# Kernel tuning notes

Measured on AMD Instinct MI355X. Metric: run time of the kernel, lower is better.

The kernel has to match this reference:

```python
import jax, jax.numpy as jnp
import numpy as np

MODEL_DIM = 1024
NUM_HEADS = 16
HEAD_DIM = MODEL_DIM // NUM_HEADS


def setup_inputs() -> dict:
    key = jax.random.key(0)
    ks = jax.random.split(key, 9)
    s = 1.0 / np.sqrt(MODEL_DIM)
    d = {
        "query": jax.random.normal(ks[0], (2, 2048, MODEL_DIM), dtype=jnp.float32),
        "Wq": jax.random.normal(ks[1], (MODEL_DIM, MODEL_DIM), dtype=jnp.float32) * s,
        "bq": jnp.zeros((MODEL_DIM,), dtype=jnp.float32),
        "Wk": jax.random.normal(ks[2], (MODEL_DIM, MODEL_DIM), dtype=jnp.float32) * s,
        "bk": jnp.zeros((MODEL_DIM,), dtype=jnp.float32),
        "Wv": jax.random.normal(ks[3], (MODEL_DIM, MODEL_DIM), dtype=jnp.float32) * s,
        "bv": jnp.zeros((MODEL_DIM,), dtype=jnp.float32),
        "Wo": jax.random.normal(ks[4], (MODEL_DIM, MODEL_DIM), dtype=jnp.float32) * s,
        "bo": jnp.zeros((MODEL_DIM,), dtype=jnp.float32),
    }
    return d


def reference(query, Wq, bq, Wk, bk, Wv, bv, Wo, bo):
    B, S, D = query.shape
    H, hd = NUM_HEADS, HEAD_DIM
    # self-attention: key = value = query
    q = (query @ Wq.T + bq).reshape(B, S, H, hd).transpose(0, 2, 1, 3)  # [B,H,S,hd]
    k = (query @ Wk.T + bk).reshape(B, S, H, hd).transpose(0, 2, 1, 3)
    v = (query @ Wv.T + bv).reshape(B, S, H, hd).transpose(0, 2, 1, 3)
    scores = jnp.einsum("bhqd,bhkd->bhqk", q, k) / np.sqrt(hd)  # [B,H,S,S]
    attn = jax.nn.softmax(scores, axis=-1)
    ctx = jnp.einsum("bhqk,bhkd->bhqd", attn, v)  # [B,H,S,hd]
    ctx = ctx.transpose(0, 2, 1, 3).reshape(B, S, D)
    return ctx @ Wo.T + bo
```

## Files before the change

kernel.cpp:

```cpp
#include <hip/hip_runtime.h>

typedef __attribute__((ext_vector_type(8))) __bf16 bf16x8;
typedef __attribute__((ext_vector_type(8))) unsigned short ushort8;
typedef __attribute__((ext_vector_type(4))) unsigned short ushort4v;
typedef __attribute__((ext_vector_type(4))) float f32x4;
typedef __attribute__((ext_vector_type(4))) _Float16 f16x4;
typedef __attribute__((ext_vector_type(8))) _Float16 f16x8;

__device__ __forceinline__ unsigned short f2bf(float f) {
    union { float f; unsigned int u; } c; c.f = f;
    unsigned int u = c.u;
    u += 0x7fffu + ((u >> 16) & 1u);
    return (unsigned short)(u >> 16);
}

__device__ __forceinline__ void async16(const void* g, void* l) {
    __builtin_amdgcn_global_load_lds(
        (const __attribute__((address_space(1))) unsigned int*)g,
        (__attribute__((address_space(3))) unsigned int*)l, 16, 0, 0);
}

__global__ __launch_bounds__(256) void cvt_all(
    const float* __restrict__ q,  const float* __restrict__ wq,
    const float* __restrict__ wk, const float* __restrict__ wv,
    const float* __restrict__ wo,
    unsigned short* __restrict__ q_bf, unsigned short* __restrict__ wqkv,
    unsigned short* __restrict__ wo_bf, float scale_k)
{
    const int NQ = 4096 * 1024, NW = 1024 * 1024;
    int i = (blockIdx.x * 256 + threadIdx.x) * 4;
    const float* src; unsigned short* dst; float sc = 1.0f; int off;
    if (i < NQ)               { src = q;  dst = q_bf;          off = i; }
    else if (i < NQ + NW)     { src = wq; dst = wqkv;          off = i - NQ; }
    else if (i < NQ + 2 * NW) { src = wk; dst = wqkv + NW;     off = i - NQ - NW; sc = scale_k; }
    else if (i < NQ + 3 * NW) { src = wv; dst = wqkv + 2 * NW; off = i - NQ - 2 * NW; }
    else                      { src = wo; dst = wo_bf;         off = i - NQ - 3 * NW; }
    float4 v = *(const float4*)(src + off);
    ushort4v o;
    o[0] = f2bf(v.x * sc); o[1] = f2bf(v.y * sc);
    o[2] = f2bf(v.z * sc); o[3] = f2bf(v.w * sc);
    *(ushort4v*)(dst + off) = o;
}

template<int MODE>
__global__ __launch_bounds__(256) void gemm_bt(
    const unsigned short* __restrict__ A,
    const unsigned short* __restrict__ B,
    void* __restrict__ Cout,
    const float* __restrict__ b0, const float* __restrict__ b1, const float* __restrict__ b2,
    float s0, float s1, float s2,
    int N, int K, int ksz)
{
    __shared__ __align__(16) unsigned short As[128 * 64];
    __shared__ __align__(16) unsigned short Bs[128 * 64];

    const int tid  = threadIdx.x;
    const int lane = tid & 63, wave = tid >> 6;
    const int quad = lane >> 4, l15 = lane & 15;
    const int wm = wave >> 1, wn = wave & 1;
    const int by = blockIdx.y, bx = blockIdx.x;
    const int k0 = blockIdx.z * ksz;

    const int srow = lane >> 3;
    const int sp   = lane & 7;
    const int scl  = sp ^ srow;
    const int sw   = l15 & 7;

    f32x4 acc[4][4];
#pragma unroll
    for (int i = 0; i < 4; ++i)
#pragma unroll
        for (int j = 0; j < 4; ++j) acc[i][j] = (f32x4)(0.0f);

    const int nk = ksz >> 6;
    for (int kt = 0; kt < nk; ++kt) {
        __syncthreads();
#pragma unroll
        for (int j = 0; j < 4; ++j) {
            int r0 = wave * 32 + j * 8;
            async16(A + (size_t)(by * 128 + r0 + srow) * K + k0 + kt * 64 + scl * 8, &As[r0 * 64]);
            async16(B + (size_t)(bx * 128 + r0 + srow) * K + k0 + kt * 64 + scl * 8, &Bs[r0 * 64]);
        }
        __syncthreads();

#pragma unroll
        for (int kh = 0; kh < 2; ++kh) {
            bf16x8 af[4], bfr[4];
#pragma unroll
            for (int mi = 0; mi < 4; ++mi)
                af[mi] = __builtin_bit_cast(bf16x8,
                    *(const ushort8*)&As[(wm * 64 + mi * 16 + l15) * 64 + ((kh * 4 + quad) ^ sw) * 8]);
#pragma unroll
            for (int ni = 0; ni < 4; ++ni)
                bfr[ni] = __builtin_bit_cast(bf16x8,
                    *(const ushort8*)&Bs[(wn * 64 + ni * 16 + l15) * 64 + ((kh * 4 + quad) ^ sw) * 8]);
#pragma unroll
            for (int mi = 0; mi < 4; ++mi)
#pragma unroll
                for (int ni = 0; ni < 4; ++ni)
                    acc[mi][ni] = __builtin_amdgcn_mfma_f32_16x16x32_bf16(af[mi], bfr[ni], acc[mi][ni], 0, 0, 0);
        }
    }

#pragma unroll
    for (int ni = 0; ni < 4; ++ni) {
        int n = bx * 128 + wn * 64 + ni * 16 + l15;
        float bias = (n < 1024) ? b0[n] * s0 : (n < 2048 ? b1[n - 1024] * s1 : b2[n - 2048] * s2);
        if (MODE == 0 && blockIdx.z != 0) bias = 0.0f;
#pragma unroll
        for (int mi = 0; mi < 4; ++mi) {
#pragma unroll
            for (int r = 0; r < 4; ++r) {
                int m = by * 128 + wm * 64 + mi * 16 + quad * 4 + r;
                float v = acc[mi][ni][r] + bias;
                if (MODE == 1) ((unsigned short*)Cout)[(size_t)m * N + n] = f2bf(v);
                else           unsafeAtomicAdd(&((float*)Cout)[(size_t)m * N + n], v);
            }
        }
    }
}

__global__ __launch_bounds__(256) void transpose_v(const unsigned short* __restrict__ qkv,
                                                   _Float16* __restrict__ vtg)
{
    __shared__ unsigned short Ls[64][68];
    const int tid = threadIdx.x;
    const int bh = blockIdx.y, st = blockIdx.x;
    const int b = bh >> 4, h = bh & 15;

#pragma unroll
    for (int i = 0; i < 2; ++i) {
        int s = tid + i * 256;
        int row = s >> 3, c8 = (s & 7) << 3;
        ushort8 v = *(const ushort8*)(qkv + (size_t)(b * 2048 + st * 64 + row) * 3072 + 2048 + h * 64 + c8);
        *(ushort8*)&Ls[row][c8] = v;
    }
    __syncthreads();
#pragma unroll
    for (int i = 0; i < 2; ++i) {
        int s = tid + i * 256;
        int hd = s >> 3, p = s & 7;
        int cl = p ^ (hd & 7);
        int g = cl >> 2, q = cl & 3;
        f16x8 o;
#pragma unroll
        for (int e = 0; e < 8; ++e) {
            int kv = g * 32 + (e >> 2) * 16 + q * 4 + (e & 3);
            union { float f; unsigned int u; } c;
            c.u = ((unsigned int)Ls[kv][hd]) << 16;
            o[e] = (_Float16)c.f;
        }
        *(f16x8*)(vtg + (size_t)(bh * 64 + hd) * 2048 + st * 64 + p * 8) = o;
    }
}

__global__ __launch_bounds__(256) void attn(const unsigned short* __restrict__ qkv,
                                            const _Float16* __restrict__ vtg,
                                            unsigned short* __restrict__ ctx)
{
    __shared__ __align__(16) unsigned short Ks[64 * 64];
    __shared__ __align__(16) _Float16 Vt[64 * 64];

    const int tid  = threadIdx.x;
    const int lane = tid & 63, wave = tid >> 6;
    const int quad = lane >> 4, l15 = lane & 15;
    const int bh = blockIdx.y;
    const int b = bh >> 4, h = bh & 15;
    const int q0 = blockIdx.x * 64;
    const int qrow = b * 2048 + q0 + wave * 16 + l15;

    const int srow = lane >> 3;
    const int sp   = lane & 7;
    const int scl  = sp ^ srow;
    const int sw   = l15 & 7;

    bf16x8 qf[2];
#pragma unroll
    for (int kh = 0; kh < 2; ++kh)
        qf[kh] = __builtin_bit_cast(bf16x8,
            *(const ushort8*)(qkv + (size_t)qrow * 3072 + h * 64 + kh * 32 + quad * 8));

    f32x4 ot[4];
#pragma unroll
    for (int ht = 0; ht < 4; ++ht) ot[ht] = (f32x4)(0.0f);
    float l_acc = 0.0f;

    for (int kt = 0; kt < 32; ++kt) {
        __syncthreads();
#pragma unroll
        for (int i = 0; i < 2; ++i) {
            int row = i * 32 + wave * 8 + srow;
            async16(qkv + (size_t)(b * 2048 + kt * 64 + row) * 3072 + 1024 + h * 64 + scl * 8,
                    &Ks[(i * 32 + wave * 8) * 64]);
            async16(vtg + (size_t)(bh * 64 + row) * 2048 + kt * 64 + sp * 8,
                    (unsigned short*)&Vt[(i * 32 + wave * 8) * 64]);
        }
        __syncthreads();

        f16x4 pv[4];
#pragma unroll
        for (int mt = 0; mt < 4; ++mt) {
            const unsigned short* kb = &Ks[(mt * 16 + l15) * 64];
            bf16x8 k0 = __builtin_bit_cast(bf16x8, *(const ushort8*)(kb + (quad ^ sw) * 8));
            bf16x8 k1 = __builtin_bit_cast(bf16x8, *(const ushort8*)(kb + ((quad ^ sw) ^ 4) * 8));
            f32x4 s4 = (f32x4)(0.0f);
            s4 = __builtin_amdgcn_mfma_f32_16x16x32_bf16(k0, qf[0], s4, 0, 0, 0);
            s4 = __builtin_amdgcn_mfma_f32_16x16x32_bf16(k1, qf[1], s4, 0, 0, 0);
#pragma unroll
            for (int r = 0; r < 4; ++r) {
                float p = __builtin_amdgcn_exp2f(s4[r]);
                l_acc += p;
                pv[mt][r] = (_Float16)p;
            }
        }

#pragma unroll
        for (int ht = 0; ht < 4; ++ht) {
            const _Float16* vb = &Vt[(ht * 16 + l15) * 64];
#pragma unroll
            for (int g = 0; g < 2; ++g) {
                f16x8 v8 = *(const f16x8*)(vb + (((g * 4 + quad) ^ sw)) * 8);
                f16x4 vlo = __builtin_shufflevector(v8, v8, 0, 1, 2, 3);
                f16x4 vhi = __builtin_shufflevector(v8, v8, 4, 5, 6, 7);
                ot[ht] = __builtin_amdgcn_mfma_f32_16x16x16f16(vlo, pv[2 * g],     ot[ht], 0, 0, 0);
                ot[ht] = __builtin_amdgcn_mfma_f32_16x16x16f16(vhi, pv[2 * g + 1], ot[ht], 0, 0, 0);
            }
        }
    }

    l_acc += __shfl_xor(l_acc, 16, 64);
    l_acc += __shfl_xor(l_acc, 32, 64);
    float inv = 1.0f / l_acc;

#pragma unroll
    for (int ht = 0; ht < 4; ++ht) {
        ushort4v o4;
#pragma unroll
        for (int r = 0; r < 4; ++r) o4[r] = f2bf(ot[ht][r] * inv);
        *(ushort4v*)(ctx + (size_t)qrow * 1024 + h * 64 + ht * 16 + quad * 4) = o4;
    }
}

extern "C" void kernel_launch(void* const* d_in, const int* in_sizes, int n_in,
                              void* d_out, int out_size, void* d_ws, size_t ws_size,
                              hipStream_t stream) {
    const float* query = (const float*)d_in[0];
    const float* Wq = (const float*)d_in[1];
    const float* bq = (const float*)d_in[2];
    const float* Wk = (const float*)d_in[3];
    const float* bk = (const float*)d_in[4];
    const float* Wv = (const float*)d_in[5];
    const float* bv = (const float*)d_in[6];
    const float* Wo = (const float*)d_in[7];
    const float* bo = (const float*)d_in[8];

    char* ws = (char*)d_ws;
    unsigned short* q_bf  = (unsigned short*)(ws);
    _Float16*       vtg   = (_Float16*)(ws);
    unsigned short* wqkv  = (unsigned short*)(ws + 8388608);
    unsigned short* wo_bf = (unsigned short*)(ws + 14680064);
    unsigned short* qkv   = (unsigned short*)(ws + 16777216);
    unsigned short* ctx   = (unsigned short*)(ws + 41943040);

    const float SCALE = 0.125f * 1.4426950408889634f;

    hipMemsetAsync(d_out, 0, (size_t)out_size * sizeof(float), stream);
    cvt_all<<<8192, 256, 0, stream>>>(query, Wq, Wk, Wv, Wo, q_bf, wqkv, wo_bf, SCALE);

    gemm_bt<1><<<dim3(24, 32), 256, 0, stream>>>(q_bf, wqkv, qkv, bq, bk, bv,
                                                 1.0f, SCALE, 1.0f, 3072, 1024, 1024);
    transpose_v<<<dim3(32, 32), 256, 0, stream>>>(qkv, vtg);
    attn<<<dim3(32, 32), 256, 0, stream>>>(qkv, vtg, ctx);
    gemm_bt<0><<<dim3(8, 32, 2), 256, 0, stream>>>(ctx, wo_bf, d_out, bo, bo, bo,
                                                   1.0f, 1.0f, 1.0f, 1024, 1024, 512);
}
```

Baseline: 222.3 us.

## Double query rows per attention block and replace split-K output GEMM with direct stores

The attention kernel now processes 128 query rows per block (two 16-row sub-tiles per wave), so each staged K/V tile is reused twice and the block count is halved. The row-sum accumulation uses packed fp16 conversion with a dot2 against ones. The output projection drops split-K with atomics and the memset in favour of a 128x64 tile kernel that writes results directly. The price is higher register pressure in attention, fp16-rounded row sums, and fewer blocks to fill the GPU.

```diff
diff --git a/kernel.cpp b/kernel.cpp
--- a/kernel.cpp
+++ b/kernel.cpp
@@ -4,8 +4,10 @@
 typedef __attribute__((ext_vector_type(8))) unsigned short ushort8;
 typedef __attribute__((ext_vector_type(4))) unsigned short ushort4v;
 typedef __attribute__((ext_vector_type(4))) float f32x4;
+typedef __attribute__((ext_vector_type(2))) _Float16 f16x2;
 typedef __attribute__((ext_vector_type(4))) _Float16 f16x4;
 typedef __attribute__((ext_vector_type(8))) _Float16 f16x8;
+typedef __attribute__((ext_vector_type(2))) __fp16 fp16v2;
 
 __device__ __forceinline__ unsigned short f2bf(float f) {
     union { float f; unsigned int u; } c; c.f = f;
@@ -42,14 +44,12 @@
     *(ushort4v*)(dst + off) = o;
 }
 
-template<int MODE>
-__global__ __launch_bounds__(256) void gemm_bt(
+__global__ __launch_bounds__(256) void qkv_gemm(
     const unsigned short* __restrict__ A,
     const unsigned short* __restrict__ B,
-    void* __restrict__ Cout,
+    unsigned short* __restrict__ Cout,
     const float* __restrict__ b0, const float* __restrict__ b1, const float* __restrict__ b2,
-    float s0, float s1, float s2,
-    int N, int K, int ksz)
+    float s1)
 {
     __shared__ __align__(16) unsigned short As[128 * 64];
     __shared__ __align__(16) unsigned short Bs[128 * 64];
@@ -59,7 +59,7 @@
     const int quad = lane >> 4, l15 = lane & 15;
     const int wm = wave >> 1, wn = wave & 1;
     const int by = blockIdx.y, bx = blockIdx.x;
-    const int k0 = blockIdx.z * ksz;
+    const int K = 1024, N = 3072;
 
     const int srow = lane >> 3;
     const int sp   = lane & 7;
@@ -72,14 +72,13 @@
 #pragma unroll
         for (int j = 0; j < 4; ++j) acc[i][j] = (f32x4)(0.0f);
 
-    const int nk = ksz >> 6;
-    for (int kt = 0; kt < nk; ++kt) {
+    for (int kt = 0; kt < 16; ++kt) {
         __syncthreads();
 #pragma unroll
         for (int j = 0; j < 4; ++j) {
             int r0 = wave * 32 + j * 8;
-            async16(A + (size_t)(by * 128 + r0 + srow) * K + k0 + kt * 64 + scl * 8, &As[r0 * 64]);
-            async16(B + (size_t)(bx * 128 + r0 + srow) * K + k0 + kt * 64 + scl * 8, &Bs[r0 * 64]);
+            async16(A + (size_t)(by * 128 + r0 + srow) * K + kt * 64 + scl * 8, &As[r0 * 64]);
+            async16(B + (size_t)(bx * 128 + r0 + srow) * K + kt * 64 + scl * 8, &Bs[r0 * 64]);
         }
         __syncthreads();
 
@@ -105,16 +104,88 @@
 #pragma unroll
     for (int ni = 0; ni < 4; ++ni) {
         int n = bx * 128 + wn * 64 + ni * 16 + l15;
-        float bias = (n < 1024) ? b0[n] * s0 : (n < 2048 ? b1[n - 1024] * s1 : b2[n - 2048] * s2);
-        if (MODE == 0 && blockIdx.z != 0) bias = 0.0f;
+        float bias = (n < 1024) ? b0[n] : (n < 2048 ? b1[n - 1024] * s1 : b2[n - 2048]);
 #pragma unroll
         for (int mi = 0; mi < 4; ++mi) {
 #pragma unroll
             for (int r = 0; r < 4; ++r) {
                 int m = by * 128 + wm * 64 + mi * 16 + quad * 4 + r;
-                float v = acc[mi][ni][r] + bias;
-                if (MODE == 1) ((unsigned short*)Cout)[(size_t)m * N + n] = f2bf(v);
-                else           unsafeAtomicAdd(&((float*)Cout)[(size_t)m * N + n], v);
+                Cout[(size_t)m * N + n] = f2bf(acc[mi][ni][r] + bias);
+            }
+        }
+    }
+}
+
+__global__ __launch_bounds__(256) void out_gemm(
+    const unsigned short* __restrict__ A,
+    const unsigned short* __restrict__ B,
+    float* __restrict__ Cout,
+    const float* __restrict__ bo)
+{
+    __shared__ __align__(16) unsigned short As[128 * 64];
+    __shared__ __align__(16) unsigned short Bs[64 * 64];
+
+    const int tid  = threadIdx.x;
+    const int lane = tid & 63, wave = tid >> 6;
+    const int quad = lane >> 4, l15 = lane & 15;
+    const int wm = wave >> 1, wn = wave & 1;
+    const int by = blockIdx.y, bx = blockIdx.x;
+    const int K = 1024;
+
+    const int srow = lane >> 3;
+    const int sp   = lane & 7;
+    const int scl  = sp ^ srow;
+    const int sw   = l15 & 7;
+
+    f32x4 acc[4][2];
+#pragma unroll
+    for (int i = 0; i < 4; ++i)
+#pragma unroll
+        for (int j = 0; j < 2; ++j) acc[i][j] = (f32x4)(0.0f);
+
+    for (int kt = 0; kt < 16; ++kt) {
+        __syncthreads();
+#pragma unroll
+        for (int j = 0; j < 4; ++j) {
+            int r0 = wave * 32 + j * 8;
+            async16(A + (size_t)(by * 128 + r0 + srow) * K + kt * 64 + scl * 8, &As[r0 * 64]);
+        }
+#pragma unroll
+        for (int j = 0; j < 2; ++j) {
+            int r0 = wave * 16 + j * 8;
+            async16(B + (size_t)(bx * 64 + r0 + srow) * K + kt * 64 + scl * 8, &Bs[r0 * 64]);
+        }
+        __syncthreads();
+
+#pragma unroll
+        for (int kh = 0; kh < 2; ++kh) {
+            bf16x8 af[4], bfr[2];
+#pragma unroll
+            for (int mi = 0; mi < 4; ++mi)
+                af[mi] = __builtin_bit_cast(bf16x8,
+                    *(const ushort8*)&As[(wm * 64 + mi * 16 + l15) * 64 + ((kh * 4 + quad) ^ sw) * 8]);
+#pragma unroll
+            for (int ni = 0; ni < 2; ++ni)
+                bfr[ni] = __builtin_bit_cast(bf16x8,
+                    *(const ushort8*)&Bs[(wn * 32 + ni * 16 + l15) * 64 + ((kh * 4 + quad) ^ sw) * 8]);
+#pragma unroll
+            for (int mi = 0; mi < 4; ++mi)
+#pragma unroll
+                for (int ni = 0; ni < 2; ++ni)
+                    acc[mi][ni] = __builtin_amdgcn_mfma_f32_16x16x32_bf16(af[mi], bfr[ni], acc[mi][ni], 0, 0, 0);
+        }
+    }
+
+#pragma unroll
+    for (int ni = 0; ni < 2; ++ni) {
+        int n = bx * 64 + wn * 32 + ni * 16 + l15;
+        float bias = bo[n];
+#pragma unroll
+        for (int mi = 0; mi < 4; ++mi) {
+#pragma unroll
+            for (int r = 0; r < 4; ++r) {
+                int m = by * 128 + wm * 64 + mi * 16 + quad * 4 + r;
+                Cout[(size_t)m * 1024 + n] = acc[mi][ni][r] + bias;
             }
         }
     }
@@ -166,24 +237,30 @@
     const int quad = lane >> 4, l15 = lane & 15;
     const int bh = blockIdx.y;
     const int b = bh >> 4, h = bh & 15;
-    const int q0 = blockIdx.x * 64;
-    const int qrow = b * 2048 + q0 + wave * 16 + l15;
+    const int q0 = blockIdx.x * 128;
 
     const int srow = lane >> 3;
     const int sp   = lane & 7;
     const int scl  = sp ^ srow;
     const int sw   = l15 & 7;
 
-    bf16x8 qf[2];
-#pragma unroll
-    for (int kh = 0; kh < 2; ++kh)
-        qf[kh] = __builtin_bit_cast(bf16x8,
-            *(const ushort8*)(qkv + (size_t)qrow * 3072 + h * 64 + kh * 32 + quad * 8));
-
-    f32x4 ot[4];
-#pragma unroll
-    for (int ht = 0; ht < 4; ++ht) ot[ht] = (f32x4)(0.0f);
-    float l_acc = 0.0f;
+    bf16x8 qf[2][2];
+#pragma unroll
+    for (int s = 0; s < 2; ++s) {
+        int qrow = b * 2048 + q0 + wave * 32 + s * 16 + l15;
+#pragma unroll
+        for (int kh = 0; kh < 2; ++kh)
+            qf[s][kh] = __builtin_bit_cast(bf16x8,
+                *(const ushort8*)(qkv + (size_t)qrow * 3072 + h * 64 + kh * 32 + quad * 8));
+    }
+
+    f32x4 ot[2][4];
+#pragma unroll
+    for (int s = 0; s < 2; ++s)
+#pragma unroll
+        for (int ht = 0; ht < 4; ++ht) ot[s][ht] = (f32x4)(0.0f);
+    float l_acc[2] = {0.0f, 0.0f};
+    const fp16v2 ones = {(__fp16)1.0f, (__fp16)1.0f};
 
     for (int kt = 0; kt < 32; ++kt) {
         __syncthreads();
@@ -197,20 +274,28 @@
         }
         __syncthreads();
 
-        f16x4 pv[4];
+        f16x4 pv[2][4];
 #pragma unroll
         for (int mt = 0; mt < 4; ++mt) {
             const unsigned short* kb = &Ks[(mt * 16 + l15) * 64];
             bf16x8 k0 = __builtin_bit_cast(bf16x8, *(const ushort8*)(kb + (quad ^ sw) * 8));
             bf16x8 k1 = __builtin_bit_cast(bf16x8, *(const ushort8*)(kb + ((quad ^ sw) ^ 4) * 8));
-            f32x4 s4 = (f32x4)(0.0f);
-            s4 = __builtin_amdgcn_mfma_f32_16x16x32_bf16(k0, qf[0], s4, 0, 0, 0);
-            s4 = __builtin_amdgcn_mfma_f32_16x16x32_bf16(k1, qf[1], s4, 0, 0, 0);
-#pragma unroll
-            for (int r = 0; r < 4; ++r) {
-                float p = __builtin_amdgcn_exp2f(s4[r]);
-                l_acc += p;
-                pv[mt][r] = (_Float16)p;
+#pragma unroll
+            for (int s = 0; s < 2; ++s) {
+                f32x4 s4 = (f32x4)(0.0f);
+                s4 = __builtin_amdgcn_mfma_f32_16x16x32_bf16(k0, qf[s][0], s4, 0, 0, 0);
+                s4 = __builtin_amdgcn_mfma_f32_16x16x32_bf16(k1, qf[s][1], s4, 0, 0, 0);
+                float p0 = __builtin_amdgcn_exp2f(s4[0]);
+                float p1 = __builtin_amdgcn_exp2f(s4[1]);
+                float p2 = __builtin_amdgcn_exp2f(s4[2]);
+                float p3 = __builtin_amdgcn_exp2f(s4[3]);
+                fp16v2 lo = __builtin_amdgcn_cvt_pkrtz(p0, p1);
+                fp16v2 hi = __builtin_amdgcn_cvt_pkrtz(p2, p3);
+                l_acc[s] = __builtin_amdgcn_fdot2(lo, ones, l_acc[s], false);
+                l_acc[s] = __builtin_amdgcn_fdot2(hi, ones, l_acc[s], false);
+                f16x2 lo2 = __builtin_bit_cast(f16x2, lo);
+                f16x2 hi2 = __builtin_bit_cast(f16x2, hi);
+                pv[s][mt] = __builtin_shufflevector(lo2, hi2, 0, 1, 2, 3);
             }
         }
 
@@ -222,22 +307,29 @@
                 f16x8 v8 = *(const f16x8*)(vb + (((g * 4 + quad) ^ sw)) * 8);
                 f16x4 vlo = __builtin_shufflevector(v8, v8, 0, 1, 2, 3);
                 f16x4 vhi = __builtin_shufflevector(v8, v8, 4, 5, 6, 7);
-                ot[ht] = __builtin_amdgcn_mfma_f32_16x16x16f16(vlo, pv[2 * g],     ot[ht], 0, 0, 0);
-                ot[ht] = __builtin_amdgcn_mfma_f32_16x16x16f16(vhi, pv[2 * g + 1], ot[ht], 0, 0, 0);
+#pragma unroll
+                for (int s = 0; s < 2; ++s) {
+                    ot[s][ht] = __builtin_amdgcn_mfma_f32_16x16x16f16(vlo, pv[s][2 * g],     ot[s][ht], 0, 0, 0);
+                    ot[s][ht] = __builtin_amdgcn_mfma_f32_16x16x16f16(vhi, pv[s][2 * g + 1], ot[s][ht], 0, 0, 0);
+                }
             }
         }
     }
 
-    l_acc += __shfl_xor(l_acc, 16, 64);
-    l_acc += __shfl_xor(l_acc, 32, 64);
-    float inv = 1.0f / l_acc;
-
-#pragma unroll
-    for (int ht = 0; ht < 4; ++ht) {
-        ushort4v o4;
-#pragma unroll
-        for (int r = 0; r < 4; ++r) o4[r] = f2bf(ot[ht][r] * inv);
-        *(ushort4v*)(ctx + (size_t)qrow * 1024 + h * 64 + ht * 16 + quad * 4) = o4;
+#pragma unroll
+    for (int s = 0; s < 2; ++s) {
+        float l = l_acc[s];
+        l += __shfl_xor(l, 16, 64);
+        l += __shfl_xor(l, 32, 64);
+        float inv = 1.0f / l;
+        int qrow = b * 2048 + q0 + wave * 32 + s * 16 + l15;
+#pragma unroll
+        for (int ht = 0; ht < 4; ++ht) {
+            ushort4v o4;
+#pragma unroll
+            for (int r = 0; r < 4; ++r) o4[r] = f2bf(ot[s][ht][r] * inv);
+            *(ushort4v*)(ctx + (size_t)qrow * 1024 + h * 64 + ht * 16 + quad * 4) = o4;
+        }
     }
 }
 
@@ -264,13 +356,9 @@
 
     const float SCALE = 0.125f * 1.4426950408889634f;
 
-    hipMemsetAsync(d_out, 0, (size_t)out_size * sizeof(float), stream);
     cvt_all<<<8192, 256, 0, stream>>>(query, Wq, Wk, Wv, Wo, q_bf, wqkv, wo_bf, SCALE);
-
-    gemm_bt<1><<<dim3(24, 32), 256, 0, stream>>>(q_bf, wqkv, qkv, bq, bk, bv,
-                                                 1.0f, SCALE, 1.0f, 3072, 1024, 1024);
+    qkv_gemm<<<dim3(24, 32), 256, 0, stream>>>(q_bf, wqkv, qkv, bq, bk, bv, SCALE);
     transpose_v<<<dim3(32, 32), 256, 0, stream>>>(qkv, vtg);
-    attn<<<dim3(32, 32), 256, 0, stream>>>(qkv, vtg, ctx);
-    gemm_bt<0><<<dim3(8, 32, 2), 256, 0, stream>>>(ctx, wo_bf, d_out, bo, bo, bo,
-                                                   1.0f, 1.0f, 1.0f, 1024, 1024, 512);
-}
+    attn<<<dim3(16, 32), 256, 0, stream>>>(qkv, vtg, ctx);
+    out_gemm<<<dim3(16, 32), 256, 0, stream>>>(ctx, wo_bf, (float*)d_out, bo);
+}
```

Result: faster. 202.9 us (-8.8%).
